# Performance work log

Measured on AMD Instinct MI355X. Metric: run time of the kernel, lower is better.

Reference implementation:

```python
import jax, jax.numpy as jnp
import numpy as np

B, T, D, H = 32, 256, 1024, 1024


def setup_inputs() -> dict:
    key = jax.random.key(0)
    ks = jax.random.split(key, 9)
    s_in = 1.0 / np.sqrt(D + H)  # torch Linear default init scale
    inp = {"x": jax.random.normal(ks[0], (B, T, D), dtype=jnp.float32)}
    names = ["f", "i", "c", "o"]
    for j, n in enumerate(names):
        # weights stored as (in_features, out_features) so we do x @ W + b
        inp[f"W{n}"] = jax.random.uniform(ks[1 + 2 * j], (D + H, H), dtype=jnp.float32,
                                          minval=-s_in, maxval=s_in)
        inp[f"b{n}"] = jax.random.uniform(ks[2 + 2 * j], (H,), dtype=jnp.float32,
                                          minval=-s_in, maxval=s_in)
    return inp


def _bilstm(x, Wf, bf, Wi, bi, Wc, bc, Wo, bo):
    # x: (B, T, D) -> time-major (T, B, D)
    xT = jnp.swapaxes(x, 0, 1)
    h0 = jnp.zeros((x.shape[0], H), dtype=x.dtype)
    c0 = jnp.zeros((x.shape[0], H), dtype=x.dtype)

    def cell(carry, xt):
        h, c = carry
        xf = jnp.concatenate([h, xt], axis=-1)  # (B, H+D): h first, matching torch cat
        f = jax.nn.sigmoid(xf @ Wf + bf)
        i = jax.nn.sigmoid(xf @ Wi + bi)
        g = jnp.tanh(xf @ Wc + bc)
        o = jax.nn.sigmoid(xf @ Wo + bo)
        c_new = f * c + i * g
        h_new = o * jnp.tanh(c_new)
        return (h_new, c_new), h_new

    _, h_fwd = jax.lax.scan(cell, (h0, c0), xT)                 # (T, B, H)
    _, h_bck = jax.lax.scan(cell, (h0, c0), xT, reverse=True)   # (T, B, H)
    out = jnp.concatenate([h_fwd, h_bck], axis=-1)              # (T, B, 2H)
    return jnp.swapaxes(out, 0, 1)                              # (B, T, 2H)


def reference(x, Wf, bf, Wi, bi, Wc, bc, Wo, bo):
    return _bilstm(x, Wf, bf, Wi, bi, Wc, bc, Wo, bo)
```

## Files before the change

### kernel.cpp

```cpp
#include <hip/hip_runtime.h>
#include <stdint.h>


typedef __attribute__((ext_vector_type(8))) short bf16x8;
typedef __attribute__((ext_vector_type(4))) float f32x4;
typedef __attribute__((ext_vector_type(16))) float f32x16;
typedef __attribute__((ext_vector_type(4))) unsigned int u32x4;

static const size_t XB_OFF  = 0;
static const size_t WXT_OFF = 16777216;
static const size_t P2_OFF  = 33554432;
static const size_t FLG_OFF = 100663296;
static const size_t FLG_SZ  = 16384;

__device__ __forceinline__ unsigned short f2bf(float f) {
    union { float f; unsigned u; } v; v.f = f;
    unsigned r = v.u + 0x7FFFu + ((v.u >> 16) & 1u);
    return (unsigned short)(r >> 16);
}
__device__ __forceinline__ float bf2f(unsigned short h) {
    union { unsigned u; float f; } v; v.u = ((unsigned)h) << 16; return v.f;
}
__device__ __forceinline__ float sigm(float x) {
    return 1.0f / (1.0f + exp2f(x * -1.4426950408889634f));
}
__device__ __forceinline__ float tanh_(float x) {
    return 1.0f - 2.0f / (1.0f + exp2f(x * 2.8853900817779268f));
}
__device__ __forceinline__ void gload16(const void* g, void* l) {
    __builtin_amdgcn_global_load_lds(
        (const __attribute__((address_space(1))) unsigned int*)g,
        (__attribute__((address_space(3))) unsigned int*)l, 16, 0, 0);
}
__device__ __forceinline__ void gstore16_sc1(void* g, u32x4 v) {
    asm volatile("global_store_dwordx4 %0, %1, off sc1" : : "v"(g), "v"(v) : "memory");
}

__global__ void k_cvt_x(const float* __restrict__ x, unsigned short* __restrict__ xb, int n) {
    int i = (blockIdx.x * blockDim.x + threadIdx.x) * 4;
    if (i < n) {
        float4 v = *(const float4*)(x + i);
        ushort4 o; o.x = f2bf(v.x); o.y = f2bf(v.y); o.z = f2bf(v.z); o.w = f2bf(v.w);
        *(ushort4*)(xb + i) = o;
    }
}

__global__ __launch_bounds__(256) void k_pack_wxt(
        const float* __restrict__ Wf, const float* __restrict__ Wi,
        const float* __restrict__ Wc, const float* __restrict__ Wo,
        unsigned short* __restrict__ wxt) {
    __shared__ unsigned short tile[64][66];
    const int k0 = blockIdx.x * 64;
    const int gate = blockIdx.y >> 4;
    const int c0 = (blockIdx.y & 15) * 64;
    const float* W = gate == 0 ? Wf : gate == 1 ? Wi : gate == 2 ? Wc : Wo;
    const int t = threadIdx.x;
    #pragma unroll
    for (int i = 0; i < 4; ++i) {
        int id = t + 256 * i;
        int r = id >> 4, fq = id & 15;
        const float* src = W + (size_t)(1024 + k0 + r) * 1024 + c0 + fq * 4;
        float4 v = *(const float4*)src;
        tile[r][fq*4+0] = f2bf(v.x); tile[r][fq*4+1] = f2bf(v.y);
        tile[r][fq*4+2] = f2bf(v.z); tile[r][fq*4+3] = f2bf(v.w);
    }
    __syncthreads();
    #pragma unroll
    for (int i = 0; i < 2; ++i) {
        int id = t + 256 * i;
        int c = id >> 3, kq = id & 7;
        ushort4 a, b;
        a.x = tile[kq*8+0][c]; a.y = tile[kq*8+1][c]; a.z = tile[kq*8+2][c]; a.w = tile[kq*8+3][c];
        b.x = tile[kq*8+4][c]; b.y = tile[kq*8+5][c]; b.z = tile[kq*8+6][c]; b.w = tile[kq*8+7][c];
        unsigned short* o = wxt + (size_t)(gate*1024 + c0 + c) * 1024 + k0 + kq*8;
        *(ushort4*)o = a;
        *((ushort4*)o + 1) = b;
    }
}

__global__ __launch_bounds__(256) void k_pgemm(
        const unsigned short* __restrict__ xb, const unsigned short* __restrict__ wxt,
        const float* __restrict__ b0, const float* __restrict__ b1,
        const float* __restrict__ b2, const float* __restrict__ b3,
        unsigned short* __restrict__ p2) {
    __shared__ char lds[32768];
    const int n0 = blockIdx.x * 128;
    const int gc0 = blockIdx.y * 128;
    const int tid = threadIdx.x;
    const int lane = tid & 63, w = tid >> 6;
    f32x16 acc[4];
    #pragma unroll
    for (int i = 0; i < 4; ++i)
        #pragma unroll
        for (int j = 0; j < 16; ++j) acc[i][j] = 0.0f;

    for (int kt = 0; kt < 16; ++kt) {
        const int k0 = kt * 64;
        #pragma unroll
        for (int i = 0; i < 4; ++i) {
            int widx = w*4 + i;
            int n = widx*64 + lane;
            int mt = n >> 8, kc = (n >> 5) & 7, r5 = n & 31;
            gload16(xb  + (size_t)(n0  + mt*32 + r5)*1024 + k0 + kc*8, lds + widx*1024);
            gload16(wxt + (size_t)(gc0 + mt*32 + r5)*1024 + k0 + kc*8, lds + 16384 + widx*1024);
        }
        __syncthreads();
        bf16x8 a[4];
        #pragma unroll
        for (int ks = 0; ks < 4; ++ks)
            a[ks] = *(const bf16x8*)(lds + w*4096 + (ks*2 + (lane>>5))*512 + (lane&31)*16);
        #pragma unroll
        for (int nt = 0; nt < 4; ++nt) {
            #pragma unroll
            for (int ks = 0; ks < 4; ++ks) {
                bf16x8 b = *(const bf16x8*)(lds + 16384 + nt*4096 + (ks*2 + (lane>>5))*512 + (lane&31)*16);
                acc[nt] = __builtin_amdgcn_mfma_f32_32x32x16_bf16(a[ks], b, acc[nt], 0, 0, 0);
            }
        }
        __syncthreads();
    }
    const int b_idx = n0 >> 8;
    const int t_base = n0 & 255;
    #pragma unroll
    for (int nt = 0; nt < 4; ++nt) {
        int gc = gc0 + nt*32 + (lane & 31);
        int gate = gc >> 10, col = gc & 1023;
        const float* bp = gate == 0 ? b0 : gate == 1 ? b1 : gate == 2 ? b2 : b3;
        float bias = bp[col];
        #pragma unroll
        for (int r = 0; r < 16; ++r) {
            int row = (r & 3) + 8*(r >> 2) + 4*(lane >> 5);
            int t = t_base + w*32 + row;
            p2[((size_t)t*32 + b_idx)*4096 + gc] = f2bf(acc[nt][r] + bias);
        }
    }
}

#define WPK   0
#define REDF  65536
#define REDB  69632
#define CSTO  73728
#define STH_H 74752
#define STH_O 75264
#define LDS_TOT 76288

extern __shared__ char smem[];

__global__ __launch_bounds__(256, 1) void k_lstm(
    const float* __restrict__ Wf, const float* __restrict__ Wi,
    const float* __restrict__ Wc, const float* __restrict__ Wo,
    const unsigned short* __restrict__ p2,
    unsigned short* __restrict__ hring,
    unsigned* __restrict__ fl,
    float* __restrict__ out)
{
    const int wg = blockIdx.x;
    const int bh = wg & 1;
    const int hc0 = (wg >> 1) * 8;
    const int tid = threadIdx.x;
    const int lane = tid & 63, w = tid >> 6;
    __shared__ int s_abort;
    if (tid == 0) s_abort = 0;

    {
        unsigned short* scr = (unsigned short*)(smem + REDF);
        const float* Wp[4] = {Wf, Wi, Wc, Wo};
        for (int blk = 0; blk < 16; ++blk) {
            int r0 = blk * 64;
            {
                int g = tid >> 6, r = tid & 63;
                const float* src = Wp[g] + (size_t)(r0 + r) * 1024 + hc0;
                float4 v0 = *(const float4*)src;
                float4 v1 = *(const float4*)(src + 4);
                unsigned short* d = scr + r*32 + g*8;
                d[0]=f2bf(v0.x); d[1]=f2bf(v0.y); d[2]=f2bf(v0.z); d[3]=f2bf(v0.w);
                d[4]=f2bf(v1.x); d[5]=f2bf(v1.y); d[6]=f2bf(v1.z); d[7]=f2bf(v1.w);
            }
            __syncthreads();
            {
                int ksl = tid >> 7, nt = (tid >> 6) & 1, l = tid & 63;
                int gcl = nt*16 + (l & 15);
                int gp = gcl >> 3, hc = gcl & 7;
                int ks = (r0 >> 5) + ksl;
                unsigned short tmp[8];
                #pragma unroll
                for (int j = 0; j < 8; ++j) {
                    int kloc = ksl*32 + (l >> 4)*8 + j;
                    tmp[j] = scr[kloc*32 + gp*8 + hc];
                }
                char* dst = smem + WPK + (size_t)((nt*32 + ks)*64 + l)*16;
                ushort4 lo, hi;
                lo.x=tmp[0]; lo.y=tmp[1]; lo.z=tmp[2]; lo.w=tmp[3];
                hi.x=tmp[4]; hi.y=tmp[5]; hi.z=tmp[6]; hi.w=tmp[7];
                *(ushort4*)dst = lo; *((ushort4*)dst + 1) = hi;
            }
            __syncthreads();
        }
    }

    for (int i = tid; i < 256; i += 256) ((float*)(smem + CSTO))[i] = 0.0f;
    const int d2 = tid >> 7, t2 = tid & 127;
    const int eb = t2 >> 3, ehc = t2 & 7;
    const int ebg = bh*16 + eb, ehcg = hc0 + ehc;
    if ((tid & 1) == 0) {
        unsigned* dst = (unsigned*)(hring + (size_t)d2*32768 + (size_t)ebg*1024 + ehcg);
        __hip_atomic_store(dst, 0u, __ATOMIC_RELAXED, __HIP_MEMORY_SCOPE_AGENT);
    }
    __syncthreads();
    if (tid == 0)
        __hip_atomic_store(fl + (size_t)bh*2048 + (wg >> 1)*16, 1u,
                           __ATOMIC_RELAXED, __HIP_MEMORY_SCOPE_AGENT);

    for (int s = 0; s < 256; ++s) {
        const int tx = d2 ? (255 - s) : s;
        const unsigned short* pp = p2 + ((size_t)tx*32 + ebg)*4096 + ehcg;
        unsigned short pf = pp[0], pi = pp[1024], pc = pp[2048], po = pp[3072];

        if (w < 2) {
            const unsigned* pw = fl + (size_t)bh*2048 + (w*64 + lane)*16;
            const unsigned tag = (unsigned)(s + 1);
            long guard = 0;
            for (;;) {
                unsigned v = __hip_atomic_load(pw, __ATOMIC_RELAXED, __HIP_MEMORY_SCOPE_AGENT);
                if (__all(v >= tag)) break;
                if (++guard >= (1L << 21)) { if (lane == 0) s_abort = 1; break; }
                __builtin_amdgcn_s_sleep(1);
            }
        }
        __syncthreads();
        if (s_abort) break;

        {
            const int nt = w & 1, kh = w >> 1;
            const unsigned short* hsF = hring + (size_t)s*65536;
            const unsigned short* hsB = hsF + 32768;
            const int row = lane & 15, kcl = lane >> 4;
            const size_t rbase = (size_t)(bh*16 + row)*1024;
            bf16x8 fF[16], fB[16];
            #pragma unroll
            for (int k8 = 0; k8 < 16; ++k8) {
                int kc = (kh*16 + k8)*4 + kcl;
                fF[k8] = *(const bf16x8*)(hsF + rbase + kc*8);
                fB[k8] = *(const bf16x8*)(hsB + rbase + kc*8);
            }
            f32x4 aF = {0.f,0.f,0.f,0.f}, aB = {0.f,0.f,0.f,0.f};
            #pragma unroll
            for (int k8 = 0; k8 < 16; ++k8) {
                int ks = kh*16 + k8;
                bf16x8 bfr = *(const bf16x8*)(smem + WPK + (size_t)((nt*32 + ks)*64 + lane)*16);
                aF = __builtin_amdgcn_mfma_f32_16x16x32_bf16(fF[k8], bfr, aF, 0, 0, 0);
                aB = __builtin_amdgcn_mfma_f32_16x16x32_bf16(fB[k8], bfr, aB, 0, 0, 0);
            }
            float* rf = (float*)(smem + REDF) + w*256;
            float* rb = (float*)(smem + REDB) + w*256;
            #pragma unroll
            for (int r = 0; r < 4; ++r) {
                int rw = (lane >> 4)*4 + r;
                rf[rw*16 + (lane & 15)] = aF[r];
                rb[rw*16 + (lane & 15)] = aB[r];
            }
        }
        __syncthreads();

        {
            const char* red = smem + (d2 ? REDB : REDF);
            float* cst = (float*)(smem + CSTO) + (size_t)(d2*16 + eb)*8 + ehc;
            unsigned short pv[4] = {pf, pi, pc, po};
            float pre[4];
            #pragma unroll
            for (int g = 0; g < 4; ++g) {
                int gc = g*8 + ehc;
                int nt = gc >> 4, col = gc & 15;
                float s0 = ((const float*)red)[nt*256 + eb*16 + col];
                float s1 = ((const float*)red)[(2 + nt)*256 + eb*16 + col];
                pre[g] = s0 + s1 + bf2f(pv[g]);
            }
            float fg = sigm(pre[0]), ig = sigm(pre[1]), gg = tanh_(pre[2]), og = sigm(pre[3]);
            float cn = fg * (*cst) + ig * gg;
            *cst = cn;
            float hv = og * tanh_(cn);
            ((unsigned short*)(smem + STH_H))[d2*128 + t2] = f2bf(hv);
            ((float*)(smem + STH_O))[d2*128 + t2] = hv;
        }
        __syncthreads();

        if (s < 255) {
            if (tid < 32) {
                int d2s = tid >> 4, ebs = tid & 15;
                u32x4 v = *(const u32x4*)(smem + STH_H + (d2s*16 + ebs)*16);
                gstore16_sc1(hring + (size_t)(s + 1)*65536 + (size_t)d2s*32768
                                   + (size_t)(bh*16 + ebs)*1024 + hc0, v);
            }
            __syncthreads();
            if (tid == 0)
                __hip_atomic_store(fl + (size_t)bh*2048 + (wg >> 1)*16, (unsigned)(s + 2),
                                   __ATOMIC_RELAXED, __HIP_MEMORY_SCOPE_AGENT);
        }

        if (tid >= 64 && tid < 128) {
            int i = tid - 64;
            int chunk = i >> 1, half = i & 1;
            int d2s = chunk >> 4, ebs = chunk & 15;
            int txs = d2s ? (255 - s) : s;
            float4 v = *(const float4*)(smem + STH_O + chunk*32 + half*16);
            *(float4*)(out + ((size_t)(bh*16 + ebs)*256 + txs)*2048
                           + (size_t)d2s*1024 + hc0 + half*4) = v;
        }
    }
}

extern "C" void kernel_launch(void* const* d_in, const int* in_sizes, int n_in,
                              void* d_out, int out_size, void* d_ws, size_t ws_size,
                              hipStream_t stream) {
    const float* x  = (const float*)d_in[0];
    const float* Wf = (const float*)d_in[1]; const float* bf_ = (const float*)d_in[2];
    const float* Wi = (const float*)d_in[3]; const float* bi_ = (const float*)d_in[4];
    const float* Wc = (const float*)d_in[5]; const float* bc_ = (const float*)d_in[6];
    const float* Wo = (const float*)d_in[7]; const float* bo_ = (const float*)d_in[8];
    char* ws = (char*)d_ws;
    unsigned short* xb    = (unsigned short*)(ws + XB_OFF);
    unsigned short* wxt   = (unsigned short*)(ws + WXT_OFF);
    unsigned short* p2    = (unsigned short*)(ws + P2_OFF);
    unsigned short* hring = (unsigned short*)(ws + XB_OFF);
    unsigned*       fl    = (unsigned*)(ws + FLG_OFF);

    hipMemsetAsync(ws + FLG_OFF, 0, FLG_SZ, stream);
    k_cvt_x<<<8192, 256, 0, stream>>>(x, xb, 32*256*1024);
    k_pack_wxt<<<dim3(16, 64), 256, 0, stream>>>(Wf, Wi, Wc, Wo, wxt);
    k_pgemm<<<dim3(64, 32), 256, 0, stream>>>(xb, wxt, bf_, bi_, bc_, bo_, p2);
    hipFuncSetAttribute((const void*)k_lstm, hipFuncAttributeMaxDynamicSharedMemorySize, LDS_TOT);
    k_lstm<<<256, 256, LDS_TOT, stream>>>(Wf, Wi, Wc, Wo, p2, hring, fl, (float*)d_out);
}
```

Before: 1.494 ms.

## Halve persistent LSTM workgroups by giving each 16 hidden columns and 512 threads

The persistent recurrent kernel now launches 128 workgroups of 512 threads instead of 256 of 256, each owning 16 hidden columns and holding twice the recurrent weight slice in LDS (about 149 KB). The flag array and per-step spin-wait shrink to 64 producers per batch half, checked by a single wave. This targets the cost of the cross-workgroup barrier each timestep, since fewer participants need to signal and be polled. In exchange each workgroup does twice the MFMA and elementwise work per step on one CU, and the LDS footprint grows substantially.

```diff
diff --git a/kernel.cpp b/kernel.cpp
--- a/kernel.cpp
+++ b/kernel.cpp
@@ -11,7 +11,7 @@
 static const size_t WXT_OFF = 16777216;
 static const size_t P2_OFF  = 33554432;
 static const size_t FLG_OFF = 100663296;
-static const size_t FLG_SZ  = 16384;
+static const size_t FLG_SZ  = 8192;
 
 __device__ __forceinline__ unsigned short f2bf(float f) {
     union { float f; unsigned u; } v; v.f = f;
@@ -137,16 +137,16 @@
 }
 
 #define WPK   0
-#define REDF  65536
-#define REDB  69632
-#define CSTO  73728
-#define STH_H 74752
-#define STH_O 75264
-#define LDS_TOT 76288
+#define REDF  131072
+#define REDB  139264
+#define CSTO  147456
+#define STH_H 149504
+#define STH_O 150528
+#define LDS_TOT 152576
 
 extern __shared__ char smem[];
 
-__global__ __launch_bounds__(256, 1) void k_lstm(
+__global__ __launch_bounds__(512, 1) void k_lstm(
     const float* __restrict__ Wf, const float* __restrict__ Wi,
     const float* __restrict__ Wc, const float* __restrict__ Wo,
     const unsigned short* __restrict__ p2,
@@ -156,7 +156,7 @@
 {
     const int wg = blockIdx.x;
     const int bh = wg & 1;
-    const int hc0 = (wg >> 1) * 8;
+    const int hc0 = (wg >> 1) * 16;
     const int tid = threadIdx.x;
     const int lane = tid & 63, w = tid >> 6;
     __shared__ int s_abort;
@@ -168,25 +168,23 @@
         for (int blk = 0; blk < 16; ++blk) {
             int r0 = blk * 64;
             {
-                int g = tid >> 6, r = tid & 63;
-                const float* src = Wp[g] + (size_t)(r0 + r) * 1024 + hc0;
+                int g = tid >> 7, rr = (tid >> 1) & 63, half = tid & 1;
+                const float* src = Wp[g] + (size_t)(r0 + rr) * 1024 + hc0 + half*8;
                 float4 v0 = *(const float4*)src;
                 float4 v1 = *(const float4*)(src + 4);
-                unsigned short* d = scr + r*32 + g*8;
+                unsigned short* d = scr + rr*64 + g*16 + half*8;
                 d[0]=f2bf(v0.x); d[1]=f2bf(v0.y); d[2]=f2bf(v0.z); d[3]=f2bf(v0.w);
                 d[4]=f2bf(v1.x); d[5]=f2bf(v1.y); d[6]=f2bf(v1.z); d[7]=f2bf(v1.w);
             }
             __syncthreads();
             {
-                int ksl = tid >> 7, nt = (tid >> 6) & 1, l = tid & 63;
-                int gcl = nt*16 + (l & 15);
-                int gp = gcl >> 3, hc = gcl & 7;
+                int nt = w & 3, ksl = w >> 2, l = lane;
                 int ks = (r0 >> 5) + ksl;
                 unsigned short tmp[8];
                 #pragma unroll
                 for (int j = 0; j < 8; ++j) {
                     int kloc = ksl*32 + (l >> 4)*8 + j;
-                    tmp[j] = scr[kloc*32 + gp*8 + hc];
+                    tmp[j] = scr[kloc*64 + nt*16 + (l & 15)];
                 }
                 char* dst = smem + WPK + (size_t)((nt*32 + ks)*64 + l)*16;
                 ushort4 lo, hi;
@@ -198,9 +196,9 @@
         }
     }
 
-    for (int i = tid; i < 256; i += 256) ((float*)(smem + CSTO))[i] = 0.0f;
-    const int d2 = tid >> 7, t2 = tid & 127;
-    const int eb = t2 >> 3, ehc = t2 & 7;
+    for (int i = tid; i < 512; i += 512) ((float*)(smem + CSTO))[i] = 0.0f;
+    const int d2 = tid >> 8, t2 = tid & 255;
+    const int eb = t2 >> 4, ehc = t2 & 15;
     const int ebg = bh*16 + eb, ehcg = hc0 + ehc;
     if ((tid & 1) == 0) {
         unsigned* dst = (unsigned*)(hring + (size_t)d2*32768 + (size_t)ebg*1024 + ehcg);
@@ -208,7 +206,7 @@
     }
     __syncthreads();
     if (tid == 0)
-        __hip_atomic_store(fl + (size_t)bh*2048 + (wg >> 1)*16, 1u,
+        __hip_atomic_store(fl + (size_t)bh*1024 + (wg >> 1)*16, 1u,
                            __ATOMIC_RELAXED, __HIP_MEMORY_SCOPE_AGENT);
 
     for (int s = 0; s < 256; ++s) {
@@ -216,8 +214,8 @@
         const unsigned short* pp = p2 + ((size_t)tx*32 + ebg)*4096 + ehcg;
         unsigned short pf = pp[0], pi = pp[1024], pc = pp[2048], po = pp[3072];
 
-        if (w < 2) {
-            const unsigned* pw = fl + (size_t)bh*2048 + (w*64 + lane)*16;
+        if (w == 0) {
+            const unsigned* pw = fl + (size_t)bh*1024 + lane*16;
             const unsigned tag = (unsigned)(s + 1);
             long guard = 0;
             for (;;) {
@@ -231,7 +229,7 @@
         if (s_abort) break;
 
         {
-            const int nt = w & 1, kh = w >> 1;
+            const int nt = w & 3, kh = w >> 2;
             const unsigned short* hsF = hring + (size_t)s*65536;
             const unsigned short* hsB = hsF + 32768;
             const int row = lane & 15, kcl = lane >> 4;
@@ -251,8 +249,8 @@
                 aF = __builtin_amdgcn_mfma_f32_16x16x32_bf16(fF[k8], bfr, aF, 0, 0, 0);
                 aB = __builtin_amdgcn_mfma_f32_16x16x32_bf16(fB[k8], bfr, aB, 0, 0, 0);
             }
-            float* rf = (float*)(smem + REDF) + w*256;
-            float* rb = (float*)(smem + REDB) + w*256;
+            float* rf = (float*)(smem + REDF) + (kh*4 + nt)*256;
+            float* rb = (float*)(smem + REDB) + (kh*4 + nt)*256;
             #pragma unroll
             for (int r = 0; r < 4; ++r) {
                 int rw = (lane >> 4)*4 + r;
@@ -263,48 +261,47 @@
         __syncthreads();
 
         {
-            const char* red = smem + (d2 ? REDB : REDF);
-            float* cst = (float*)(smem + CSTO) + (size_t)(d2*16 + eb)*8 + ehc;
+            const float* red = (const float*)(smem + (d2 ? REDB : REDF));
+            float* cst = (float*)(smem + CSTO) + (size_t)(d2*16 + eb)*16 + ehc;
             unsigned short pv[4] = {pf, pi, pc, po};
             float pre[4];
             #pragma unroll
             for (int g = 0; g < 4; ++g) {
-                int gc = g*8 + ehc;
-                int nt = gc >> 4, col = gc & 15;
-                float s0 = ((const float*)red)[nt*256 + eb*16 + col];
-                float s1 = ((const float*)red)[(2 + nt)*256 + eb*16 + col];
+                float s0 = red[(0*4 + g)*256 + eb*16 + ehc];
+                float s1 = red[(1*4 + g)*256 + eb*16 + ehc];
                 pre[g] = s0 + s1 + bf2f(pv[g]);
             }
             float fg = sigm(pre[0]), ig = sigm(pre[1]), gg = tanh_(pre[2]), og = sigm(pre[3]);
             float cn = fg * (*cst) + ig * gg;
             *cst = cn;
             float hv = og * tanh_(cn);
-            ((unsigned short*)(smem + STH_H))[d2*128 + t2] = f2bf(hv);
-            ((float*)(smem + STH_O))[d2*128 + t2] = hv;
+            ((unsigned short*)(smem + STH_H))[d2*256 + t2] = f2bf(hv);
+            ((float*)(smem + STH_O))[d2*256 + t2] = hv;
         }
         __syncthreads();
 
         if (s < 255) {
-            if (tid < 32) {
-                int d2s = tid >> 4, ebs = tid & 15;
-                u32x4 v = *(const u32x4*)(smem + STH_H + (d2s*16 + ebs)*16);
+            if (tid < 64) {
+                int chunk = tid >> 1, half = tid & 1;
+                int d2s = chunk >> 4, ebs = chunk & 15;
+                u32x4 v = *(const u32x4*)(smem + STH_H + chunk*32 + half*16);
                 gstore16_sc1(hring + (size_t)(s + 1)*65536 + (size_t)d2s*32768
-                                   + (size_t)(bh*16 + ebs)*1024 + hc0, v);
+                                   + (size_t)(bh*16 + ebs)*1024 + hc0 + half*8, v);
             }
             __syncthreads();
             if (tid == 0)
-                __hip_atomic_store(fl + (size_t)bh*2048 + (wg >> 1)*16, (unsigned)(s + 2),
+                __hip_atomic_store(fl + (size_t)bh*1024 + (wg >> 1)*16, (unsigned)(s + 2),
                                    __ATOMIC_RELAXED, __HIP_MEMORY_SCOPE_AGENT);
         }
 
-        if (tid >= 64 && tid < 128) {
+        if (tid >= 64 && tid < 192) {
             int i = tid - 64;
-            int chunk = i >> 1, half = i & 1;
+            int chunk = i >> 2, q = i & 3;
             int d2s = chunk >> 4, ebs = chunk & 15;
             int txs = d2s ? (255 - s) : s;
-            float4 v = *(const float4*)(smem + STH_O + chunk*32 + half*16);
+            float4 v = *(const float4*)(smem + STH_O + chunk*64 + q*16);
             *(float4*)(out + ((size_t)(bh*16 + ebs)*256 + txs)*2048
-                           + (size_t)d2s*1024 + hc0 + half*4) = v;
+                           + (size_t)d2s*1024 + hc0 + q*4) = v;
         }
     }
 }
@@ -329,5 +326,5 @@
     k_pack_wxt<<<dim3(16, 64), 256, 0, stream>>>(Wf, Wi, Wc, Wo, wxt);
     k_pgemm<<<dim3(64, 32), 256, 0, stream>>>(xb, wxt, bf_, bi_, bc_, bo_, p2);
     hipFuncSetAttribute((const void*)k_lstm, hipFuncAttributeMaxDynamicSharedMemorySize, LDS_TOT);
-    k_lstm<<<256, 256, LDS_TOT, stream>>>(Wf, Wi, Wc, Wo, p2, hring, fl, (float*)d_out);
-}
+    k_lstm<<<128, 512, LDS_TOT, stream>>>(Wf, Wi, Wc, Wo, p2, hring, fl, (float*)d_out);
+}
```

After: 2.395 ms. 1.6x slower.
